# Kernel tuning notes

Hardware: AMD Instinct MI355X
Metric: run time of the kernel (lower is better)

## Reference

```python
import jax, jax.numpy as jnp
import numpy as np

NUM_NODES = 12
NUM_EDGES = 30
OUT_CH = 32
HID = 192
B = 8192
FEAT = 2 * (NUM_NODES - 1)            # 22
N = B * NUM_NODES                      # 98304 nodes
E = B * NUM_EDGES                      # 245760 edges
OUT_SPACE = NUM_NODES ** 2 - NUM_NODES # 132


def setup_inputs() -> dict:
    key = jax.random.key(0)
    ks = jax.random.split(key, 16)
    def p(k, shape, fan):
        return jax.random.normal(k, shape, dtype=jnp.float32) / np.float32(np.sqrt(fan))
    return {
        "x": jax.random.normal(ks[0], (N, FEAT), dtype=jnp.float32),
        "edge_attr": jax.random.normal(ks[1], (E, NUM_EDGES), dtype=jnp.float32),
        "edge_index": jax.random.randint(ks[2], (2, E), 0, N, dtype=jnp.int64) if jax.config.jax_enable_x64 else jax.random.randint(ks[2], (2, E), 0, N, dtype=jnp.int32),
        "mlp1_w1": p(ks[3], (NUM_EDGES, HID), NUM_EDGES),
        "mlp1_b1": jnp.zeros((HID,), jnp.float32),
        "mlp1_w2": p(ks[4], (HID, FEAT * OUT_CH), HID),
        "mlp1_b2": jnp.zeros((FEAT * OUT_CH,), jnp.float32),
        "root1": p(ks[5], (FEAT, OUT_CH), FEAT),
        "bias1": jnp.zeros((OUT_CH,), jnp.float32),
        "lin1_w": p(ks[6], (NUM_NODES * OUT_CH, 96), NUM_NODES * OUT_CH),
        "lin1_b": jnp.zeros((96,), jnp.float32),
        "lin2_w": p(ks[7], (96, 48), 96),
        "lin2_b": jnp.zeros((48,), jnp.float32),
        "lin3_w": p(ks[8], (48, OUT_SPACE), 48),
        "lin3_b": jnp.zeros((OUT_SPACE,), jnp.float32),
    }


def reference(x, edge_attr, edge_index, mlp1_w1, mlp1_b1, mlp1_w2, mlp1_b2,
              root1, bias1, lin1_w, lin1_b, lin2_w, lin2_b, lin3_w, lin3_b):
    src, dst = edge_index[0], edge_index[1]
    # Edge-MLP ('Understanding'): produces a [FEAT, OUT_CH] weight per edge
    h = jax.nn.relu(edge_attr @ mlp1_w1 + mlp1_b1)               # [E, HID]
    W = (h @ mlp1_w2 + mlp1_b2).reshape(-1, FEAT, OUT_CH)        # [E, 22, 32]
    # NNConv: gather source features, per-edge matmul, scatter-add to dst
    msg = jnp.einsum('ec,eco->eo', x[src], W)                    # [E, 32]
    agg = jax.ops.segment_sum(msg, dst, num_segments=x.shape[0]) # [N, 32]
    g = jax.nn.relu(x @ root1 + agg + bias1)                     # conv1 + ReLU
    # Dense head
    g = g.reshape(-1, NUM_NODES * OUT_CH)                        # [B, 384]
    g = jax.nn.relu(g @ lin1_w + lin1_b)
    g = jax.nn.relu(g @ lin2_w + lin2_b)
    g = jax.nn.relu(g @ lin3_w + lin3_b)                         # [B, 132]
    return g
```

## Files before the change

kernel.cpp:

```cpp
#include <hip/hip_runtime.h>
#include <hip/hip_bf16.h>

typedef short s8v __attribute__((ext_vector_type(8)));
typedef float f4v __attribute__((ext_vector_type(4)));

#define MFMA16(A,B,C) __builtin_amdgcn_mfma_f32_16x16x32_bf16((A),(B),(C),0,0,0)

#define E_TOT 245760
#define N_TOT 98304

__device__ __forceinline__ unsigned short f2bf(float f) {
    unsigned u = __builtin_bit_cast(unsigned, f);
    u += 0x7fffu + ((u >> 16) & 1u);
    return (unsigned short)(u >> 16);
}
__device__ __forceinline__ float bflo(unsigned u) {
    return __builtin_bit_cast(float, u << 16);
}
__device__ __forceinline__ float bfhi(unsigned u) {
    return __builtin_bit_cast(float, u & 0xffff0000u);
}
__device__ __forceinline__ void gload_lds16(const void* g, void* l) {
    __builtin_amdgcn_global_load_lds(
        (const __attribute__((address_space(1))) void*)g,
        (__attribute__((address_space(3))) void*)l, 16, 0, 0);
}

__global__ void pack_kernel(const float* __restrict__ w1, const float* __restrict__ w2,
                            const float* __restrict__ l1w, const float* __restrict__ l2w,
                            const float* __restrict__ l3w,
                            unsigned short* __restrict__ w1p, unsigned short* __restrict__ w2p,
                            unsigned short* __restrict__ l1p, unsigned short* __restrict__ l2p,
                            unsigned short* __restrict__ l3p)
{
    int idx = blockIdx.x * 256 + threadIdx.x;
    if (idx >= 192000) return;
    if (idx < 6144) {
        int i = idx & 7, l = (idx >> 3) & 63, nt = idx >> 9;
        int k = (l >> 4) * 8 + i, col = nt * 16 + (l & 15);
        w1p[idx] = f2bf(k < 30 ? w1[k * 192 + col] : 0.f);
    } else if (idx < 141312) {
        int e = idx - 6144;
        int i = e & 7, l = (e >> 3) & 63, rest = e >> 9;
        int s = rest % 6, ct = rest / 6, t = ct & 1, c = ct >> 1;
        int k = s * 32 + (l >> 4) * 8 + i, j = c * 32 + t * 16 + (l & 15);
        w2p[e] = f2bf(w2[k * 704 + j]);
    } else if (idx < 178176) {
        int e = idx - 141312;
        int i = e & 7, l = (e >> 3) & 63, rest = e >> 9;
        int s = rest % 12, nt = rest / 12;
        int k = s * 32 + (l >> 4) * 8 + i, j = nt * 16 + (l & 15);
        l1p[e] = f2bf(l1w[k * 96 + j]);
    } else if (idx < 182784) {
        int e = idx - 178176;
        int i = e & 7, l = (e >> 3) & 63, rest = e >> 9;
        int s = rest % 3, nt = rest / 3;
        int k = s * 32 + (l >> 4) * 8 + i, j = nt * 16 + (l & 15);
        l2p[e] = f2bf(l2w[k * 48 + j]);
    } else {
        int e = idx - 182784;
        int i = e & 7, l = (e >> 3) & 63, rest = e >> 9;
        int s = rest & 1, nt = rest >> 1;
        int k = s * 32 + (l >> 4) * 8 + i, j = nt * 16 + (l & 15);
        l3p[e] = f2bf((k < 48 && j < 132) ? l3w[k * 132 + j] : 0.f);
    }
}

__launch_bounds__(256, 3)
__global__ void edge_kernel(const float* __restrict__ x,
                            const float* __restrict__ ea,
                            const int*   __restrict__ eidx,
                            const unsigned short* __restrict__ w1p,
                            const unsigned short* __restrict__ w2p,
                            const float* __restrict__ b1,
                            const float* __restrict__ b2,
                            float* __restrict__ agg)
{
    __shared__ __align__(16) unsigned char smem[38400];
    unsigned short* w2u  = (unsigned short*)smem;
    unsigned short* hscr = (unsigned short*)smem;
    unsigned short* xs   = (unsigned short*)(smem + 25600);
    float*          b2l  = (float*)(smem + 34816);
    int*            dstl = (int*)(smem + 37632);

    const int tid  = threadIdx.x;
    const int wave = tid >> 6, lane = tid & 63;
    const int hi = lane >> 4, col = lane & 15;
    const int e0 = blockIdx.x * 192;

    for (int idx = tid; idx < 192 * 22; idx += 256) {
        int e = idx / 22, c = idx - e * 22;
        int s = eidx[e0 + e];
        xs[e * 24 + c] = f2bf(x[s * 22 + c]);
    }
    for (int idx = tid; idx < 192; idx += 256) dstl[idx] = eidx[E_TOT + e0 + idx];
    for (int idx = tid; idx < 704; idx += 256) b2l[idx] = b2[idx];

    s8v w1f[12];
#pragma unroll
    for (int nt = 0; nt < 12; ++nt) w1f[nt] = *(const s8v*)(w1p + (nt * 64 + lane) * 8);
    float b1v[12];
#pragma unroll
    for (int nt = 0; nt < 12; ++nt) b1v[nt] = b1[nt * 16 + col];

    s8v haf[3][6];
#pragma unroll
    for (int mt = 0; mt < 3; ++mt) {
        int er = e0 + wave * 48 + mt * 16 + col;
        s8v af;
#pragma unroll
        for (int i = 0; i < 8; ++i) {
            int k = hi * 8 + i;
            af[i] = (short)f2bf(k < 30 ? ea[er * 30 + k] : 0.f);
        }
        f4v hc[12];
#pragma unroll
        for (int nt = 0; nt < 12; ++nt) {
            f4v z = {0.f, 0.f, 0.f, 0.f};
            hc[nt] = MFMA16(af, w1f[nt], z);
        }
#pragma unroll
        for (int nt = 0; nt < 12; ++nt)
#pragma unroll
            for (int r = 0; r < 4; ++r) {
                float v = hc[nt][r] + b1v[nt];
                v = v > 0.f ? v : 0.f;
                hscr[(wave * 16 + hi * 4 + r) * 200 + nt * 16 + col] = f2bf(v);
            }
#pragma unroll
        for (int s = 0; s < 6; ++s)
            haf[mt][s] = *(const s8v*)&hscr[(wave * 16 + col) * 200 + s * 32 + hi * 8];
    }

    __syncthreads();

#pragma unroll
    for (int r = 0; r < 3; ++r)
        gload_lds16(w2p + (r * 256 + tid) * 8, w2u + (r * 256 + wave * 64) * 8);
    __syncthreads();

    f4v msg[3][2];
#pragma unroll
    for (int mt = 0; mt < 3; ++mt)
#pragma unroll
        for (int t = 0; t < 2; ++t) msg[mt][t] = (f4v){0.f, 0.f, 0.f, 0.f};

    for (int cp = 0; cp < 11; ++cp) {
        {
            const int c = 2 * cp;
#pragma unroll
            for (int r = 0; r < 3; ++r)
                gload_lds16(w2p + (c + 1) * 6144 + (r * 256 + tid) * 8,
                            w2u + 6144 + (r * 256 + wave * 64) * 8);
            f4v pacc[3][2];
#pragma unroll
            for (int t = 0; t < 2; ++t) {
                float bv = b2l[c * 32 + t * 16 + col];
#pragma unroll
                for (int mt = 0; mt < 3; ++mt) pacc[mt][t] = (f4v){bv, bv, bv, bv};
#pragma unroll
                for (int s = 0; s < 6; ++s) {
                    s8v bfr = *(const s8v*)&w2u[((t * 6 + s) * 64 + lane) * 8];
#pragma unroll
                    for (int mt = 0; mt < 3; ++mt)
                        pacc[mt][t] = MFMA16(haf[mt][s], bfr, pacc[mt][t]);
                }
            }
#pragma unroll
            for (int mt = 0; mt < 3; ++mt)
#pragma unroll
                for (int r = 0; r < 4; ++r) {
                    unsigned xu = *(const unsigned*)&xs[(wave * 48 + mt * 16 + hi * 4 + r) * 24 + c];
                    float xv = bflo(xu);
                    msg[mt][0][r] += xv * pacc[mt][0][r];
                    msg[mt][1][r] += xv * pacc[mt][1][r];
                }
            __syncthreads();
        }
        {
            const int c = 2 * cp + 1;
            if (c < 21) {
#pragma unroll
                for (int r = 0; r < 3; ++r)
                    gload_lds16(w2p + (c + 1) * 6144 + (r * 256 + tid) * 8,
                                w2u + (r * 256 + wave * 64) * 8);
            }
            f4v pacc[3][2];
#pragma unroll
            for (int t = 0; t < 2; ++t) {
                float bv = b2l[c * 32 + t * 16 + col];
#pragma unroll
                for (int mt = 0; mt < 3; ++mt) pacc[mt][t] = (f4v){bv, bv, bv, bv};
#pragma unroll
                for (int s = 0; s < 6; ++s) {
                    s8v bfr = *(const s8v*)&w2u[6144 + ((t * 6 + s) * 64 + lane) * 8];
#pragma unroll
                    for (int mt = 0; mt < 3; ++mt)
                        pacc[mt][t] = MFMA16(haf[mt][s], bfr, pacc[mt][t]);
                }
            }
#pragma unroll
            for (int mt = 0; mt < 3; ++mt)
#pragma unroll
                for (int r = 0; r < 4; ++r) {
                    unsigned xu = *(const unsigned*)&xs[(wave * 48 + mt * 16 + hi * 4 + r) * 24 + c - 1];
                    float xv = bfhi(xu);
                    msg[mt][0][r] += xv * pacc[mt][0][r];
                    msg[mt][1][r] += xv * pacc[mt][1][r];
                }
            __syncthreads();
        }
    }

#pragma unroll
    for (int mt = 0; mt < 3; ++mt)
#pragma unroll
        for (int r = 0; r < 4; ++r) {
            int e = wave * 48 + mt * 16 + hi * 4 + r;
            int d = dstl[e];
            atomicAdd(&agg[d * 32 + col],      msg[mt][0][r]);
            atomicAdd(&agg[d * 32 + 16 + col], msg[mt][1][r]);
        }
}

__launch_bounds__(256)
__global__ void node_kernel(const float* __restrict__ x, const float* __restrict__ agg,
                            const float* __restrict__ root1, const float* __restrict__ bias1,
                            unsigned short* __restrict__ g2d)
{
    const int tid = threadIdx.x, wave = tid >> 6, lane = tid & 63;
    const int hi = lane >> 4, col = lane & 15;
    const int n0 = blockIdx.x * 256 + wave * 64;

    s8v bfr[2];
#pragma unroll
    for (int nt = 0; nt < 2; ++nt)
#pragma unroll
        for (int i = 0; i < 8; ++i) {
            int k = hi * 8 + i;
            bfr[nt][i] = (short)f2bf(k < 22 ? root1[k * 32 + nt * 16 + col] : 0.f);
        }
    float bb0 = bias1[col], bb1 = bias1[16 + col];

#pragma unroll
    for (int mt = 0; mt < 4; ++mt) {
        int node = n0 + mt * 16 + col;
        s8v af;
        if (hi < 2) {
            const float2* p = (const float2*)&x[node * 22 + hi * 8];
            float2 t0 = p[0], t1 = p[1], t2 = p[2], t3 = p[3];
            af[0] = (short)f2bf(t0.x); af[1] = (short)f2bf(t0.y);
            af[2] = (short)f2bf(t1.x); af[3] = (short)f2bf(t1.y);
            af[4] = (short)f2bf(t2.x); af[5] = (short)f2bf(t2.y);
            af[6] = (short)f2bf(t3.x); af[7] = (short)f2bf(t3.y);
        } else if (hi == 2) {
            const float2* p = (const float2*)&x[node * 22 + 16];
            float2 t0 = p[0], t1 = p[1], t2 = p[2];
            af[0] = (short)f2bf(t0.x); af[1] = (short)f2bf(t0.y);
            af[2] = (short)f2bf(t1.x); af[3] = (short)f2bf(t1.y);
            af[4] = (short)f2bf(t2.x); af[5] = (short)f2bf(t2.y);
            af[6] = 0; af[7] = 0;
        } else {
            af = (s8v)0;
        }
        f4v c0 = {bb0, bb0, bb0, bb0};
        f4v c1 = {bb1, bb1, bb1, bb1};
        c0 = MFMA16(af, bfr[0], c0);
        c1 = MFMA16(af, bfr[1], c1);
#pragma unroll
        for (int r = 0; r < 4; ++r) {
            int row = n0 + mt * 16 + hi * 4 + r;
            float v0 = c0[r] + agg[row * 32 + col];
            float v1 = c1[r] + agg[row * 32 + 16 + col];
            g2d[row * 32 + col]      = f2bf(v0 > 0.f ? v0 : 0.f);
            g2d[row * 32 + 16 + col] = f2bf(v1 > 0.f ? v1 : 0.f);
        }
    }
}

__launch_bounds__(256)
__global__ void head_kernel(const unsigned short* __restrict__ g2d,
                            const unsigned short* __restrict__ l1p,
                            const unsigned short* __restrict__ l2p,
                            const unsigned short* __restrict__ l3p,
                            const float* __restrict__ l1b,
                            const float* __restrict__ l2b,
                            const float* __restrict__ l3b,
                            float* __restrict__ out)
{
    __shared__ __align__(16) unsigned short a1s[4][16][104];
    __shared__ __align__(16) unsigned short a2s[4][16][56];

    const int tid = threadIdx.x, wave = tid >> 6, lane = tid & 63;
    const int hi = lane >> 4, col = lane & 15;
    const int r0 = blockIdx.x * 64 + wave * 16;

    f4v acc1[6];
#pragma unroll
    for (int nt = 0; nt < 6; ++nt) {
        float bv = l1b[nt * 16 + col];
        acc1[nt] = (f4v){bv, bv, bv, bv};
    }
#pragma unroll
    for (int s = 0; s < 12; ++s) {
        s8v a = *(const s8v*)&g2d[(r0 + col) * 384 + s * 32 + hi * 8];
#pragma unroll
        for (int nt = 0; nt < 6; ++nt) {
            s8v b = *(const s8v*)&l1p[((nt * 12 + s) * 64 + lane) * 8];
            acc1[nt] = MFMA16(a, b, acc1[nt]);
        }
    }
#pragma unroll
    for (int nt = 0; nt < 6; ++nt)
#pragma unroll
        for (int r = 0; r < 4; ++r) {
            float v = acc1[nt][r];
            a1s[wave][hi * 4 + r][nt * 16 + col] = f2bf(v > 0.f ? v : 0.f);
        }

    f4v acc2[3];
#pragma unroll
    for (int nt = 0; nt < 3; ++nt) {
        float bv = l2b[nt * 16 + col];
        acc2[nt] = (f4v){bv, bv, bv, bv};
    }
#pragma unroll
    for (int s = 0; s < 3; ++s) {
        s8v a = *(const s8v*)&a1s[wave][col][s * 32 + hi * 8];
#pragma unroll
        for (int nt = 0; nt < 3; ++nt) {
            s8v b = *(const s8v*)&l2p[((nt * 3 + s) * 64 + lane) * 8];
            acc2[nt] = MFMA16(a, b, acc2[nt]);
        }
    }
#pragma unroll
    for (int nt = 0; nt < 3; ++nt)
#pragma unroll
        for (int r = 0; r < 4; ++r) {
            float v = acc2[nt][r];
            a2s[wave][hi * 4 + r][nt * 16 + col] = f2bf(v > 0.f ? v : 0.f);
        }

    f4v acc3[9];
#pragma unroll
    for (int nt = 0; nt < 9; ++nt) {
        int oc = nt * 16 + col;
        float bv = oc < 132 ? l3b[oc] : 0.f;
        acc3[nt] = (f4v){bv, bv, bv, bv};
    }
#pragma unroll
    for (int s = 0; s < 2; ++s) {
        s8v a;
        if (s == 1 && hi >= 2) a = (s8v)0;
        else a = *(const s8v*)&a2s[wave][col][s * 32 + hi * 8];
#pragma unroll
        for (int nt = 0; nt < 9; ++nt) {
            s8v b = *(const s8v*)&l3p[((nt * 2 + s) * 64 + lane) * 8];
            acc3[nt] = MFMA16(a, b, acc3[nt]);
        }
    }
#pragma unroll
    for (int nt = 0; nt < 9; ++nt) {
        int oc = nt * 16 + col;
        if (oc < 132) {
#pragma unroll
            for (int r = 0; r < 4; ++r) {
                float v = acc3[nt][r];
                out[(r0 + hi * 4 + r) * 132 + oc] = v > 0.f ? v : 0.f;
            }
        }
    }
}

extern "C" void kernel_launch(void* const* d_in, const int* in_sizes, int n_in,
                              void* d_out, int out_size, void* d_ws, size_t ws_size,
                              hipStream_t stream)
{
    const float* x     = (const float*)d_in[0];
    const float* ea    = (const float*)d_in[1];
    const int*   ei    = (const int*)d_in[2];
    const float* w1    = (const float*)d_in[3];
    const float* b1    = (const float*)d_in[4];
    const float* w2    = (const float*)d_in[5];
    const float* b2    = (const float*)d_in[6];
    const float* root1 = (const float*)d_in[7];
    const float* bias1 = (const float*)d_in[8];
    const float* l1w   = (const float*)d_in[9];
    const float* l1b   = (const float*)d_in[10];
    const float* l2w   = (const float*)d_in[11];
    const float* l2b   = (const float*)d_in[12];
    const float* l3w   = (const float*)d_in[13];
    const float* l3b   = (const float*)d_in[14];
    float* out = (float*)d_out;

    char* ws = (char*)d_ws;
    unsigned short* w1p = (unsigned short*)(ws + 0);
    unsigned short* w2p = (unsigned short*)(ws + 12288);
    unsigned short* l1p = (unsigned short*)(ws + 282624);
    unsigned short* l2p = (unsigned short*)(ws + 356352);
    unsigned short* l3p = (unsigned short*)(ws + 365568);
    float*          agg = (float*)(ws + 384000);
    unsigned short* g2d = (unsigned short*)(ws + 12966912);

    hipMemsetAsync(agg, 0, (size_t)N_TOT * 32 * 4, stream);
    pack_kernel<<<750, 256, 0, stream>>>(w1, w2, l1w, l2w, l3w, w1p, w2p, l1p, l2p, l3p);
    edge_kernel<<<1280, 256, 0, stream>>>(x, ea, ei, w1p, w2p, b1, b2, agg);
    node_kernel<<<384, 256, 0, stream>>>(x, agg, root1, bias1, g2d);
    head_kernel<<<128, 256, 0, stream>>>(g2d, l1p, l2p, l3p, l1b, l2b, l3b, out);
}
```

Measured before the change: 214.4 us.

## Fuse root term into agg init, merge prep kernels, shrink edge tiles

The memset is removed and the node kernel is folded into the weight-pack kernel: extra blocks write x@root1+bias1 straight into agg, so the edge atomics add on top of it. The head kernel now applies ReLU and the bf16 conversion while staging agg into LDS, so the g2d intermediate buffer is no longer needed. The edge kernel drops to 128 edges per block at occupancy 4 with a compact xs layout and vectorized x gathers. The head kernel handles 8 rows per wave, which leaves half the MFMA lanes idle, in exchange for twice as many blocks.

```diff
diff --git a/kernel.cpp b/kernel.cpp
--- a/kernel.cpp
+++ b/kernel.cpp
@@ -26,211 +26,54 @@
         (__attribute__((address_space(3))) void*)l, 16, 0, 0);
 }
 
-__global__ void pack_kernel(const float* __restrict__ w1, const float* __restrict__ w2,
+__launch_bounds__(256)
+__global__ void prep_kernel(const float* __restrict__ w1, const float* __restrict__ w2,
                             const float* __restrict__ l1w, const float* __restrict__ l2w,
                             const float* __restrict__ l3w,
                             unsigned short* __restrict__ w1p, unsigned short* __restrict__ w2p,
                             unsigned short* __restrict__ l1p, unsigned short* __restrict__ l2p,
-                            unsigned short* __restrict__ l3p)
+                            unsigned short* __restrict__ l3p,
+                            const float* __restrict__ x, const float* __restrict__ root1,
+                            const float* __restrict__ bias1, float* __restrict__ agg)
 {
-    int idx = blockIdx.x * 256 + threadIdx.x;
-    if (idx >= 192000) return;
-    if (idx < 6144) {
-        int i = idx & 7, l = (idx >> 3) & 63, nt = idx >> 9;
-        int k = (l >> 4) * 8 + i, col = nt * 16 + (l & 15);
-        w1p[idx] = f2bf(k < 30 ? w1[k * 192 + col] : 0.f);
-    } else if (idx < 141312) {
-        int e = idx - 6144;
-        int i = e & 7, l = (e >> 3) & 63, rest = e >> 9;
-        int s = rest % 6, ct = rest / 6, t = ct & 1, c = ct >> 1;
-        int k = s * 32 + (l >> 4) * 8 + i, j = c * 32 + t * 16 + (l & 15);
-        w2p[e] = f2bf(w2[k * 704 + j]);
-    } else if (idx < 178176) {
-        int e = idx - 141312;
-        int i = e & 7, l = (e >> 3) & 63, rest = e >> 9;
-        int s = rest % 12, nt = rest / 12;
-        int k = s * 32 + (l >> 4) * 8 + i, j = nt * 16 + (l & 15);
-        l1p[e] = f2bf(l1w[k * 96 + j]);
-    } else if (idx < 182784) {
-        int e = idx - 178176;
-        int i = e & 7, l = (e >> 3) & 63, rest = e >> 9;
-        int s = rest % 3, nt = rest / 3;
-        int k = s * 32 + (l >> 4) * 8 + i, j = nt * 16 + (l & 15);
-        l2p[e] = f2bf(l2w[k * 48 + j]);
-    } else {
-        int e = idx - 182784;
-        int i = e & 7, l = (e >> 3) & 63, rest = e >> 9;
-        int s = rest & 1, nt = rest >> 1;
-        int k = s * 32 + (l >> 4) * 8 + i, j = nt * 16 + (l & 15);
-        l3p[e] = f2bf((k < 48 && j < 132) ? l3w[k * 132 + j] : 0.f);
-    }
-}
-
-__launch_bounds__(256, 3)
-__global__ void edge_kernel(const float* __restrict__ x,
-                            const float* __restrict__ ea,
-                            const int*   __restrict__ eidx,
-                            const unsigned short* __restrict__ w1p,
-                            const unsigned short* __restrict__ w2p,
-                            const float* __restrict__ b1,
-                            const float* __restrict__ b2,
-                            float* __restrict__ agg)
-{
-    __shared__ __align__(16) unsigned char smem[38400];
-    unsigned short* w2u  = (unsigned short*)smem;
-    unsigned short* hscr = (unsigned short*)smem;
-    unsigned short* xs   = (unsigned short*)(smem + 25600);
-    float*          b2l  = (float*)(smem + 34816);
-    int*            dstl = (int*)(smem + 37632);
-
-    const int tid  = threadIdx.x;
-    const int wave = tid >> 6, lane = tid & 63;
-    const int hi = lane >> 4, col = lane & 15;
-    const int e0 = blockIdx.x * 192;
-
-    for (int idx = tid; idx < 192 * 22; idx += 256) {
-        int e = idx / 22, c = idx - e * 22;
-        int s = eidx[e0 + e];
-        xs[e * 24 + c] = f2bf(x[s * 22 + c]);
-    }
-    for (int idx = tid; idx < 192; idx += 256) dstl[idx] = eidx[E_TOT + e0 + idx];
-    for (int idx = tid; idx < 704; idx += 256) b2l[idx] = b2[idx];
-
-    s8v w1f[12];
-#pragma unroll
-    for (int nt = 0; nt < 12; ++nt) w1f[nt] = *(const s8v*)(w1p + (nt * 64 + lane) * 8);
-    float b1v[12];
-#pragma unroll
-    for (int nt = 0; nt < 12; ++nt) b1v[nt] = b1[nt * 16 + col];
-
-    s8v haf[3][6];
-#pragma unroll
-    for (int mt = 0; mt < 3; ++mt) {
-        int er = e0 + wave * 48 + mt * 16 + col;
-        s8v af;
-#pragma unroll
-        for (int i = 0; i < 8; ++i) {
-            int k = hi * 8 + i;
-            af[i] = (short)f2bf(k < 30 ? ea[er * 30 + k] : 0.f);
-        }
-        f4v hc[12];
-#pragma unroll
-        for (int nt = 0; nt < 12; ++nt) {
-            f4v z = {0.f, 0.f, 0.f, 0.f};
-            hc[nt] = MFMA16(af, w1f[nt], z);
-        }
-#pragma unroll
-        for (int nt = 0; nt < 12; ++nt)
-#pragma unroll
-            for (int r = 0; r < 4; ++r) {
-                float v = hc[nt][r] + b1v[nt];
-                v = v > 0.f ? v : 0.f;
-                hscr[(wave * 16 + hi * 4 + r) * 200 + nt * 16 + col] = f2bf(v);
-            }
-#pragma unroll
-        for (int s = 0; s < 6; ++s)
-            haf[mt][s] = *(const s8v*)&hscr[(wave * 16 + col) * 200 + s * 32 + hi * 8];
-    }
-
-    __syncthreads();
-
-#pragma unroll
-    for (int r = 0; r < 3; ++r)
-        gload_lds16(w2p + (r * 256 + tid) * 8, w2u + (r * 256 + wave * 64) * 8);
-    __syncthreads();
-
-    f4v msg[3][2];
-#pragma unroll
-    for (int mt = 0; mt < 3; ++mt)
-#pragma unroll
-        for (int t = 0; t < 2; ++t) msg[mt][t] = (f4v){0.f, 0.f, 0.f, 0.f};
-
-    for (int cp = 0; cp < 11; ++cp) {
-        {
-            const int c = 2 * cp;
-#pragma unroll
-            for (int r = 0; r < 3; ++r)
-                gload_lds16(w2p + (c + 1) * 6144 + (r * 256 + tid) * 8,
-                            w2u + 6144 + (r * 256 + wave * 64) * 8);
-            f4v pacc[3][2];
-#pragma unroll
-            for (int t = 0; t < 2; ++t) {
-                float bv = b2l[c * 32 + t * 16 + col];
-#pragma unroll
-                for (int mt = 0; mt < 3; ++mt) pacc[mt][t] = (f4v){bv, bv, bv, bv};
-#pragma unroll
-                for (int s = 0; s < 6; ++s) {
-                    s8v bfr = *(const s8v*)&w2u[((t * 6 + s) * 64 + lane) * 8];
-#pragma unroll
-                    for (int mt = 0; mt < 3; ++mt)
-                        pacc[mt][t] = MFMA16(haf[mt][s], bfr, pacc[mt][t]);
-                }
-            }
-#pragma unroll
-            for (int mt = 0; mt < 3; ++mt)
-#pragma unroll
-                for (int r = 0; r < 4; ++r) {
-                    unsigned xu = *(const unsigned*)&xs[(wave * 48 + mt * 16 + hi * 4 + r) * 24 + c];
-                    float xv = bflo(xu);
-                    msg[mt][0][r] += xv * pacc[mt][0][r];
-                    msg[mt][1][r] += xv * pacc[mt][1][r];
-                }
-            __syncthreads();
-        }
-        {
-            const int c = 2 * cp + 1;
-            if (c < 21) {
-#pragma unroll
-                for (int r = 0; r < 3; ++r)
-                    gload_lds16(w2p + (c + 1) * 6144 + (r * 256 + tid) * 8,
-                                w2u + (r * 256 + wave * 64) * 8);
-            }
-            f4v pacc[3][2];
-#pragma unroll
-            for (int t = 0; t < 2; ++t) {
-                float bv = b2l[c * 32 + t * 16 + col];
-#pragma unroll
-                for (int mt = 0; mt < 3; ++mt) pacc[mt][t] = (f4v){bv, bv, bv, bv};
-#pragma unroll
-                for (int s = 0; s < 6; ++s) {
-                    s8v bfr = *(const s8v*)&w2u[6144 + ((t * 6 + s) * 64 + lane) * 8];
-#pragma unroll
-                    for (int mt = 0; mt < 3; ++mt)
-                        pacc[mt][t] = MFMA16(haf[mt][s], bfr, pacc[mt][t]);
-                }
-            }
-#pragma unroll
-            for (int mt = 0; mt < 3; ++mt)
-#pragma unroll
-                for (int r = 0; r < 4; ++r) {
-                    unsigned xu = *(const unsigned*)&xs[(wave * 48 + mt * 16 + hi * 4 + r) * 24 + c - 1];
-                    float xv = bfhi(xu);
-                    msg[mt][0][r] += xv * pacc[mt][0][r];
-                    msg[mt][1][r] += xv * pacc[mt][1][r];
-                }
-            __syncthreads();
-        }
-    }
-
-#pragma unroll
-    for (int mt = 0; mt < 3; ++mt)
-#pragma unroll
-        for (int r = 0; r < 4; ++r) {
-            int e = wave * 48 + mt * 16 + hi * 4 + r;
-            int d = dstl[e];
-            atomicAdd(&agg[d * 32 + col],      msg[mt][0][r]);
-            atomicAdd(&agg[d * 32 + 16 + col], msg[mt][1][r]);
-        }
-}
-
-__launch_bounds__(256)
-__global__ void node_kernel(const float* __restrict__ x, const float* __restrict__ agg,
-                            const float* __restrict__ root1, const float* __restrict__ bias1,
-                            unsigned short* __restrict__ g2d)
-{
+    if (blockIdx.x < 750) {
+        int idx = blockIdx.x * 256 + threadIdx.x;
+        if (idx >= 192000) return;
+        if (idx < 6144) {
+            int i = idx & 7, l = (idx >> 3) & 63, nt = idx >> 9;
+            int k = (l >> 4) * 8 + i, col = nt * 16 + (l & 15);
+            w1p[idx] = f2bf(k < 30 ? w1[k * 192 + col] : 0.f);
+        } else if (idx < 141312) {
+            int e = idx - 6144;
+            int i = e & 7, l = (e >> 3) & 63, rest = e >> 9;
+            int s = rest % 6, ct = rest / 6, t = ct & 1, c = ct >> 1;
+            int k = s * 32 + (l >> 4) * 8 + i, j = c * 32 + t * 16 + (l & 15);
+            w2p[e] = f2bf(w2[k * 704 + j]);
+        } else if (idx < 178176) {
+            int e = idx - 141312;
+            int i = e & 7, l = (e >> 3) & 63, rest = e >> 9;
+            int s = rest % 12, nt = rest / 12;
+            int k = s * 32 + (l >> 4) * 8 + i, j = nt * 16 + (l & 15);
+            l1p[e] = f2bf(l1w[k * 96 + j]);
+        } else if (idx < 182784) {
+            int e = idx - 178176;
+            int i = e & 7, l = (e >> 3) & 63, rest = e >> 9;
+            int s = rest % 3, nt = rest / 3;
+            int k = s * 32 + (l >> 4) * 8 + i, j = nt * 16 + (l & 15);
+            l2p[e] = f2bf(l2w[k * 48 + j]);
+        } else {
+            int e = idx - 182784;
+            int i = e & 7, l = (e >> 3) & 63, rest = e >> 9;
+            int s = rest & 1, nt = rest >> 1;
+            int k = s * 32 + (l >> 4) * 8 + i, j = nt * 16 + (l & 15);
+            l3p[e] = f2bf((k < 48 && j < 132) ? l3w[k * 132 + j] : 0.f);
+        }
+        return;
+    }
+
     const int tid = threadIdx.x, wave = tid >> 6, lane = tid & 63;
     const int hi = lane >> 4, col = lane & 15;
-    const int n0 = blockIdx.x * 256 + wave * 64;
+    const int n0 = (blockIdx.x - 750) * 256 + wave * 64;
 
     s8v bfr[2];
 #pragma unroll
@@ -270,16 +113,179 @@
 #pragma unroll
         for (int r = 0; r < 4; ++r) {
             int row = n0 + mt * 16 + hi * 4 + r;
-            float v0 = c0[r] + agg[row * 32 + col];
-            float v1 = c1[r] + agg[row * 32 + 16 + col];
-            g2d[row * 32 + col]      = f2bf(v0 > 0.f ? v0 : 0.f);
-            g2d[row * 32 + 16 + col] = f2bf(v1 > 0.f ? v1 : 0.f);
-        }
-    }
+            agg[row * 32 + col]      = c0[r];
+            agg[row * 32 + 16 + col] = c1[r];
+        }
+    }
+}
+
+__launch_bounds__(256, 4)
+__global__ void edge_kernel(const float* __restrict__ x,
+                            const float* __restrict__ ea,
+                            const int*   __restrict__ eidx,
+                            const unsigned short* __restrict__ w1p,
+                            const unsigned short* __restrict__ w2p,
+                            const float* __restrict__ b1,
+                            const float* __restrict__ b2,
+                            float* __restrict__ agg)
+{
+    __shared__ __align__(16) unsigned char smem[34560];
+    unsigned short* w2c  = (unsigned short*)smem;
+    unsigned short* hscr = (unsigned short*)smem;
+    unsigned short* xs   = (unsigned short*)(smem + 25600);
+    float*          b2l  = (float*)(smem + 31232);
+    int*            dstl = (int*)(smem + 34048);
+
+    const int tid  = threadIdx.x;
+    const int wave = tid >> 6, lane = tid & 63;
+    const int hi = lane >> 4, col = lane & 15;
+    const int e0 = blockIdx.x * 128;
+
+    if (tid < 128) {
+        int s = eidx[e0 + tid];
+        dstl[tid] = eidx[E_TOT + e0 + tid];
+        const float2* p = (const float2*)&x[s * 22];
+#pragma unroll
+        for (int c2 = 0; c2 < 11; ++c2) {
+            float2 v = p[c2];
+            unsigned pk = (unsigned)f2bf(v.x) | ((unsigned)f2bf(v.y) << 16);
+            *(unsigned*)&xs[tid * 22 + 2 * c2] = pk;
+        }
+    }
+    for (int idx = tid; idx < 704; idx += 256) b2l[idx] = b2[idx];
+
+    s8v w1f[12];
+#pragma unroll
+    for (int nt = 0; nt < 12; ++nt) w1f[nt] = *(const s8v*)(w1p + (nt * 64 + lane) * 8);
+    float b1v[12];
+#pragma unroll
+    for (int nt = 0; nt < 12; ++nt) b1v[nt] = b1[nt * 16 + col];
+
+    s8v haf[2][6];
+#pragma unroll
+    for (int mt = 0; mt < 2; ++mt) {
+        int er = e0 + wave * 32 + mt * 16 + col;
+        s8v af;
+#pragma unroll
+        for (int i = 0; i < 8; ++i) {
+            int k = hi * 8 + i;
+            af[i] = (short)f2bf(k < 30 ? ea[er * 30 + k] : 0.f);
+        }
+        f4v hc[12];
+#pragma unroll
+        for (int nt = 0; nt < 12; ++nt) {
+            f4v z = {0.f, 0.f, 0.f, 0.f};
+            hc[nt] = MFMA16(af, w1f[nt], z);
+        }
+#pragma unroll
+        for (int nt = 0; nt < 12; ++nt)
+#pragma unroll
+            for (int r = 0; r < 4; ++r) {
+                float v = hc[nt][r] + b1v[nt];
+                v = v > 0.f ? v : 0.f;
+                hscr[(wave * 16 + hi * 4 + r) * 200 + nt * 16 + col] = f2bf(v);
+            }
+#pragma unroll
+        for (int s = 0; s < 6; ++s)
+            haf[mt][s] = *(const s8v*)&hscr[(wave * 16 + col) * 200 + s * 32 + hi * 8];
+    }
+
+    __syncthreads();
+
+#pragma unroll
+    for (int r = 0; r < 3; ++r)
+        gload_lds16(w2p + (r * 256 + tid) * 8, w2c + (r * 256 + wave * 64) * 8);
+    __syncthreads();
+
+    f4v msg[2][2];
+#pragma unroll
+    for (int mt = 0; mt < 2; ++mt)
+#pragma unroll
+        for (int t = 0; t < 2; ++t) msg[mt][t] = (f4v){0.f, 0.f, 0.f, 0.f};
+
+    for (int cp = 0; cp < 11; ++cp) {
+        unsigned xu[8];
+#pragma unroll
+        for (int mt = 0; mt < 2; ++mt)
+#pragma unroll
+            for (int r = 0; r < 4; ++r)
+                xu[mt * 4 + r] = *(const unsigned*)&xs[(wave * 32 + mt * 16 + hi * 4 + r) * 22 + 2 * cp];
+
+        {
+            const int c = 2 * cp;
+#pragma unroll
+            for (int r = 0; r < 3; ++r)
+                gload_lds16(w2p + (c + 1) * 6144 + (r * 256 + tid) * 8,
+                            w2c + 6144 + (r * 256 + wave * 64) * 8);
+            f4v pacc[2][2];
+#pragma unroll
+            for (int t = 0; t < 2; ++t) {
+                float bv = b2l[c * 32 + t * 16 + col];
+                pacc[0][t] = (f4v){bv, bv, bv, bv};
+                pacc[1][t] = (f4v){bv, bv, bv, bv};
+#pragma unroll
+                for (int s = 0; s < 6; ++s) {
+                    s8v bfr = *(const s8v*)&w2c[((t * 6 + s) * 64 + lane) * 8];
+                    pacc[0][t] = MFMA16(haf[0][s], bfr, pacc[0][t]);
+                    pacc[1][t] = MFMA16(haf[1][s], bfr, pacc[1][t]);
+                }
+            }
+#pragma unroll
+            for (int mt = 0; mt < 2; ++mt)
+#pragma unroll
+                for (int r = 0; r < 4; ++r) {
+                    float xv = bflo(xu[mt * 4 + r]);
+                    msg[mt][0][r] += xv * pacc[mt][0][r];
+                    msg[mt][1][r] += xv * pacc[mt][1][r];
+                }
+            __syncthreads();
+        }
+        {
+            const int c = 2 * cp + 1;
+            if (c < 21) {
+#pragma unroll
+                for (int r = 0; r < 3; ++r)
+                    gload_lds16(w2p + (c + 1) * 6144 + (r * 256 + tid) * 8,
+                                w2c + (r * 256 + wave * 64) * 8);
+            }
+            f4v pacc[2][2];
+#pragma unroll
+            for (int t = 0; t < 2; ++t) {
+                float bv = b2l[c * 32 + t * 16 + col];
+                pacc[0][t] = (f4v){bv, bv, bv, bv};
+                pacc[1][t] = (f4v){bv, bv, bv, bv};
+#pragma unroll
+                for (int s = 0; s < 6; ++s) {
+                    s8v bfr = *(const s8v*)&w2c[6144 + ((t * 6 + s) * 64 + lane) * 8];
+                    pacc[0][t] = MFMA16(haf[0][s], bfr, pacc[0][t]);
+                    pacc[1][t] = MFMA16(haf[1][s], bfr, pacc[1][t]);
+                }
+            }
+#pragma unroll
+            for (int mt = 0; mt < 2; ++mt)
+#pragma unroll
+                for (int r = 0; r < 4; ++r) {
+                    float xv = bfhi(xu[mt * 4 + r]);
+                    msg[mt][0][r] += xv * pacc[mt][0][r];
+                    msg[mt][1][r] += xv * pacc[mt][1][r];
+                }
+            __syncthreads();
+        }
+    }
+
+#pragma unroll
+    for (int mt = 0; mt < 2; ++mt)
+#pragma unroll
+        for (int r = 0; r < 4; ++r) {
+            int e = wave * 32 + mt * 16 + hi * 4 + r;
+            int d = dstl[e];
+            atomicAdd(&agg[d * 32 + col],      msg[mt][0][r]);
+            atomicAdd(&agg[d * 32 + 16 + col], msg[mt][1][r]);
+        }
 }
 
 __launch_bounds__(256)
-__global__ void head_kernel(const unsigned short* __restrict__ g2d,
+__global__ void head_kernel(const float* __restrict__ agg,
                             const unsigned short* __restrict__ l1p,
                             const unsigned short* __restrict__ l2p,
                             const unsigned short* __restrict__ l3p,
@@ -288,12 +294,27 @@
                             const float* __restrict__ l3b,
                             float* __restrict__ out)
 {
-    __shared__ __align__(16) unsigned short a1s[4][16][104];
-    __shared__ __align__(16) unsigned short a2s[4][16][56];
+    __shared__ __align__(16) unsigned short gls[4 * 8 * 392];
+    __shared__ __align__(16) unsigned short a1s[4 * 8 * 104];
+    __shared__ __align__(16) unsigned short a2s[4 * 8 * 56];
 
     const int tid = threadIdx.x, wave = tid >> 6, lane = tid & 63;
-    const int hi = lane >> 4, col = lane & 15;
-    const int r0 = blockIdx.x * 64 + wave * 16;
+    const int hi = lane >> 4, col = lane & 15, c8 = col & 7;
+    const int r0 = blockIdx.x * 32 + wave * 8;
+
+    const f4v* a4 = (const f4v*)(agg + (size_t)r0 * 384);
+#pragma unroll
+    for (int it = 0; it < 12; ++it) {
+        int q = it * 64 + lane;
+        f4v v = a4[q];
+#pragma unroll
+        for (int j = 0; j < 4; ++j) v[j] = v[j] > 0.f ? v[j] : 0.f;
+        int row = q / 96, coloff = (q - row * 96) * 4;
+        unsigned pk0 = (unsigned)f2bf(v[0]) | ((unsigned)f2bf(v[1]) << 16);
+        unsigned pk1 = (unsigned)f2bf(v[2]) | ((unsigned)f2bf(v[3]) << 16);
+        *(unsigned*)&gls[(wave * 8 + row) * 392 + coloff]     = pk0;
+        *(unsigned*)&gls[(wave * 8 + row) * 392 + coloff + 2] = pk1;
+    }
 
     f4v acc1[6];
 #pragma unroll
@@ -303,20 +324,22 @@
     }
 #pragma unroll
     for (int s = 0; s < 12; ++s) {
-        s8v a = *(const s8v*)&g2d[(r0 + col) * 384 + s * 32 + hi * 8];
+        s8v a = *(const s8v*)&gls[(wave * 8 + c8) * 392 + s * 32 + hi * 8];
 #pragma unroll
         for (int nt = 0; nt < 6; ++nt) {
             s8v b = *(const s8v*)&l1p[((nt * 12 + s) * 64 + lane) * 8];
             acc1[nt] = MFMA16(a, b, acc1[nt]);
         }
     }
-#pragma unroll
-    for (int nt = 0; nt < 6; ++nt)
-#pragma unroll
-        for (int r = 0; r < 4; ++r) {
-            float v = acc1[nt][r];
-            a1s[wave][hi * 4 + r][nt * 16 + col] = f2bf(v > 0.f ? v : 0.f);
-        }
+    if (hi < 2) {
+#pragma unroll
+        for (int nt = 0; nt < 6; ++nt)
+#pragma unroll
+            for (int r = 0; r < 4; ++r) {
+                float v = acc1[nt][r];
+                a1s[(wave * 8 + hi * 4 + r) * 104 + nt * 16 + col] = f2bf(v > 0.f ? v : 0.f);
+            }
+    }
 
     f4v acc2[3];
 #pragma unroll
@@ -326,20 +349,22 @@
     }
 #pragma unroll
     for (int s = 0; s < 3; ++s) {
-        s8v a = *(const s8v*)&a1s[wave][col][s * 32 + hi * 8];
+        s8v a = *(const s8v*)&a1s[(wave * 8 + c8) * 104 + s * 32 + hi * 8];
 #pragma unroll
         for (int nt = 0; nt < 3; ++nt) {
             s8v b = *(const s8v*)&l2p[((nt * 3 + s) * 64 + lane) * 8];
             acc2[nt] = MFMA16(a, b, acc2[nt]);
         }
     }
-#pragma unroll
-    for (int nt = 0; nt < 3; ++nt)
-#pragma unroll
-        for (int r = 0; r < 4; ++r) {
-            float v = acc2[nt][r];
-            a2s[wave][hi * 4 + r][nt * 16 + col] = f2bf(v > 0.f ? v : 0.f);
-        }
+    if (hi < 2) {
+#pragma unroll
+        for (int nt = 0; nt < 3; ++nt)
+#pragma unroll
+            for (int r = 0; r < 4; ++r) {
+                float v = acc2[nt][r];
+                a2s[(wave * 8 + hi * 4 + r) * 56 + nt * 16 + col] = f2bf(v > 0.f ? v : 0.f);
+            }
+    }
 
     f4v acc3[9];
 #pragma unroll
@@ -352,21 +377,23 @@
     for (int s = 0; s < 2; ++s) {
         s8v a;
         if (s == 1 && hi >= 2) a = (s8v)0;
-        else a = *(const s8v*)&a2s[wave][col][s * 32 + hi * 8];
+        else a = *(const s8v*)&a2s[(wave * 8 + c8) * 56 + s * 32 + hi * 8];
 #pragma unroll
         for (int nt = 0; nt < 9; ++nt) {
             s8v b = *(const s8v*)&l3p[((nt * 2 + s) * 64 + lane) * 8];
             acc3[nt] = MFMA16(a, b, acc3[nt]);
         }
     }
-#pragma unroll
-    for (int nt = 0; nt < 9; ++nt) {
-        int oc = nt * 16 + col;
-        if (oc < 132) {
-#pragma unroll
-            for (int r = 0; r < 4; ++r) {
-                float v = acc3[nt][r];
-                out[(r0 + hi * 4 + r) * 132 + oc] = v > 0.f ? v : 0.f;
+    if (hi < 2) {
+#pragma unroll
+        for (int nt = 0; nt < 9; ++nt) {
+            int oc = nt * 16 + col;
+            if (oc < 132) {
+#pragma unroll
+                for (int r = 0; r < 4; ++r) {
+                    float v = acc3[nt][r];
+                    out[(r0 + hi * 4 + r) * 132 + oc] = v > 0.f ? v : 0.f;
+                }
             }
         }
     }
@@ -400,11 +427,9 @@
     unsigned short* l2p = (unsigned short*)(ws + 356352);
     unsigned short* l3p = (unsigned short*)(ws + 365568);
     float*          agg = (float*)(ws + 384000);
-    unsigned short* g2d = (unsigned short*)(ws + 12966912);
-
-    hipMemsetAsync(agg, 0, (size_t)N_TOT * 32 * 4, stream);
-    pack_kernel<<<750, 256, 0, stream>>>(w1, w2, l1w, l2w, l3w, w1p, w2p, l1p, l2p, l3p);
-    edge_kernel<<<1280, 256, 0, stream>>>(x, ea, ei, w1p, w2p, b1, b2, agg);
-    node_kernel<<<384, 256, 0, stream>>>(x, agg, root1, bias1, g2d);
-    head_kernel<<<128, 256, 0, stream>>>(g2d, l1p, l2p, l3p, l1b, l2b, l3b, out);
-}
+
+    prep_kernel<<<1134, 256, 0, stream>>>(w1, w2, l1w, l2w, l3w, w1p, w2p, l1p, l2p, l3p,
+                                          x, root1, bias1, agg);
+    edge_kernel<<<1920, 256, 0, stream>>>(x, ea, ei, w1p, w2p, b1, b2, agg);
+    head_kernel<<<256, 256, 0, stream>>>(agg, l1p, l2p, l3p, l1b, l2b, l3b, out);
+}
```

After: 209.3 us. -2.4%, faster.
